# Kernel optimization log

Measured on AMD Instinct MI355X. Metric: run time of the kernel, lower is better.

Reference implementation:

```python
import jax, jax.numpy as jnp
import numpy as np

B, H, W, C = 8, 56, 56, 2048
NUM_HEADS = 8
WINDOW = 7  # partition/merge is identity for this per-token op; kept for documentation
D = C // NUM_HEADS  # 256


def setup_inputs() -> dict:
    key = jax.random.key(0)
    kx, kw = jax.random.split(key)
    x = jax.random.normal(kx, (B, H, W, C), dtype=jnp.float32)
    # per-head square weight, as in nn.Parameter(torch.randn(num_heads, d, d))
    weight = jax.random.normal(kw, (NUM_HEADS, D, D), dtype=jnp.float32)
    return {"x": x, "weight": weight}


def reference(x, weight):
    # Swin-style window partition -> per-head linear on each token -> window merge.
    # Partition and merge are exact inverse layout permutations, so the math
    # reduces to a per-token, per-head d x d matmul over the channel dim.
    b, h, w, c = x.shape
    n_heads, d, _ = weight.shape
    xh = x.reshape(b, h, w, n_heads, d)
    out = jnp.einsum('bhwnd,nde->bhwne', xh, weight)  # grouped small GEMM
    return out.reshape(b, h, w, c)
```

## Files before the change

### kernel.cpp

```cpp
#include <hip/hip_runtime.h>
#include <hip/hip_bf16.h>
#include <cstdint>

typedef __attribute__((ext_vector_type(8))) short v8s;
typedef __attribute__((ext_vector_type(4))) float v4f;

#define NUM_HEADS 8
#define D 256
#define CCH 2048
#define SEGS 64

__device__ __forceinline__ short f2bf(float f) {
  unsigned u = __builtin_bit_cast(unsigned, f);
  u = (u + 0x7FFFu + ((u >> 16) & 1u)) >> 16;
  return (short)u;
}

__global__ __launch_bounds__(256) void pack_w(const float* __restrict__ w,
                                              short* __restrict__ p) {
  int idx  = blockIdx.x * 256 + threadIdx.x;
  int lane = idx & 63;
  int j    = (idx >> 6) & 15;
  int s    = (idx >> 10) & 7;
  int head = idx >> 13;
  int n  = j * 16 + (lane & 15);
  int k0 = s * 32 + (lane >> 4) * 8;
  const float* src = w + head * 65536 + k0 * 256 + n;
  v8s v;
#pragma unroll
  for (int e = 0; e < 8; ++e) v[e] = f2bf(src[e * 256]);
  *reinterpret_cast<v8s*>(p + (size_t)idx * 8) = v;
}

typedef __attribute__((address_space(1))) const unsigned int GAS;
typedef __attribute__((address_space(3))) unsigned int LAS;

__global__ __launch_bounds__(512, 4) void grouped_mm(const float* __restrict__ x,
                                                     const short* __restrict__ pB,
                                                     float* __restrict__ out) {
  __shared__ alignas(16) char As[3][16384];
  const int tid  = threadIdx.x;
  const int wv   = tid >> 6;
  const int lane = tid & 63;
  const int head = blockIdx.x >> 6;
  const int seg  = blockIdx.x & 63;
  const int t0   = (seg < 32) ? seg * 25 : 800 + (seg - 32) * 24;
  const int nt   = (seg < 32) ? 25 : 24;

  const int arow = lane & 15;
  const int kg   = lane >> 4;

  v8s Bf0[8], Bf1[8];
  {
    const short* pb = pB + (size_t)head * 65536 + (size_t)lane * 8;
#pragma unroll
    for (int s = 0; s < 8; ++s) {
      Bf0[s] = *reinterpret_cast<const v8s*>(pb + (size_t)(s * 16 + 2 * wv)     * 512);
      Bf1[s] = *reinterpret_cast<const v8s*>(pb + (size_t)(s * 16 + 2 * wv + 1) * 512);
    }
  }

  const char* xbase = (const char*)(x + (size_t)head * D);

  auto stage = [&](int slot, int t) {
#pragma unroll
    for (int q = 0; q < 2; ++q) {
      const int r = 2 * wv + q;
      const unsigned lsw = ((unsigned)(lane * 16)) ^ (unsigned)((r & 7) << 4);
      const char* g = xbase + ((size_t)(t * 16 + r)) * (CCH * 4) + lsw;
      char* l = &As[0][0] + slot * 16384 + r * 1024;
      __builtin_amdgcn_global_load_lds((GAS*)g, (LAS*)l, 16, 0, 0);
    }
  };

  stage(0, t0);
  stage(1, t0 + 1);
  asm volatile("s_waitcnt vmcnt(2)" ::: "memory");
  __builtin_amdgcn_s_barrier();

  const unsigned rswz = (unsigned)((arow & 7) << 4);
  int cur = 0;

  for (int p = 0; p < nt; ++p) {
    int nslot = cur + 2; if (nslot >= 3) nslot -= 3;
    if (p + 2 < nt) stage(nslot, t0 + p + 2);

    const char* ar = &As[0][0] + cur * 16384 + arow * 1024;
    v4f acc0 = (v4f){0.f, 0.f, 0.f, 0.f};
    v4f acc1 = (v4f){0.f, 0.f, 0.f, 0.f};
#pragma unroll
    for (int s = 0; s < 8; ++s) {
      const unsigned q0 = ((unsigned)(s * 128 + kg * 32)) ^ rswz;
      v4f lo = *reinterpret_cast<const v4f*>(ar + q0);
      v4f hi = *reinterpret_cast<const v4f*>(ar + (q0 ^ 16u));
      v8s af;
#pragma unroll
      for (int e = 0; e < 4; ++e) {
        af[e]     = f2bf(lo[e]);
        af[4 + e] = f2bf(hi[e]);
      }
      acc0 = __builtin_amdgcn_mfma_f32_16x16x32_bf16(af, Bf0[s], acc0, 0, 0, 0);
      acc1 = __builtin_amdgcn_mfma_f32_16x16x32_bf16(af, Bf1[s], acc1, 0, 0, 0);
    }

    float* op = out + (size_t)((t0 + p) * 16 + kg * 4) * CCH
                    + head * D + wv * 32 + arow;
#pragma unroll
    for (int r = 0; r < 4; ++r) {
      op[(size_t)r * CCH]      = acc0[r];
      op[(size_t)r * CCH + 16] = acc1[r];
    }

    asm volatile("s_waitcnt vmcnt(10)" ::: "memory");
    __builtin_amdgcn_s_barrier();

    cur = cur + 1; if (cur >= 3) cur = 0;
  }
}

extern "C" void kernel_launch(void* const* d_in, const int* in_sizes, int n_in,
                              void* d_out, int out_size, void* d_ws, size_t ws_size,
                              hipStream_t stream) {
  const float* x = (const float*)d_in[0];
  const float* w = (const float*)d_in[1];
  float* out = (float*)d_out;
  short* packed = (short*)d_ws;

  pack_w<<<256, 256, 0, stream>>>(w, packed);
  grouped_mm<<<NUM_HEADS * SEGS, 512, 0, stream>>>(x, packed, out);
}
```

Baseline: 89.15 us.

## Stage activations through registers, convert to bf16 once before LDS

Replaces the direct global-to-LDS fp32 staging with register loads. Each thread converts its slice to bf16 once and writes it into a half-sized swizzled LDS tile. Before, every wave re-converted the same fp32 A tile, so this removes redundant conversions and halves LDS footprint and read traffic. In exchange, the prefetch now passes through VGPRs with a manually unrolled double-register pipeline. The vmcnt waits also cover outstanding output stores, which may add stalls in a kernel that is already near memory bandwidth.

```diff
diff --git a/kernel.cpp b/kernel.cpp
--- a/kernel.cpp
+++ b/kernel.cpp
@@ -32,13 +32,10 @@
   *reinterpret_cast<v8s*>(p + (size_t)idx * 8) = v;
 }
 
-typedef __attribute__((address_space(1))) const unsigned int GAS;
-typedef __attribute__((address_space(3))) unsigned int LAS;
-
 __global__ __launch_bounds__(512, 4) void grouped_mm(const float* __restrict__ x,
                                                      const short* __restrict__ pB,
                                                      float* __restrict__ out) {
-  __shared__ alignas(16) char As[3][16384];
+  __shared__ alignas(16) char As[3][8192];
   const int tid  = threadIdx.x;
   const int wv   = tid >> 6;
   const int lane = tid & 63;
@@ -47,8 +44,8 @@
   const int t0   = (seg < 32) ? seg * 25 : 800 + (seg - 32) * 24;
   const int nt   = (seg < 32) ? 25 : 24;
 
-  const int arow = lane & 15;
-  const int kg   = lane >> 4;
+  const int row = lane & 15;
+  const int kg  = lane >> 4;
 
   v8s Bf0[8], Bf1[8];
   {
@@ -60,62 +57,74 @@
     }
   }
 
-  const char* xbase = (const char*)(x + (size_t)head * D);
+  const int srow  = tid >> 5;
+  const int skseg = tid & 31;
+  const unsigned swoff = (unsigned)(srow * 512)
+                       + (((unsigned)(skseg * 16)) ^ ((unsigned)((srow & 7) << 4)));
+  const float* xbase = x + (size_t)head * D + (size_t)srow * CCH + skseg * 8;
 
-  auto stage = [&](int slot, int t) {
+  auto issue = [&](int t, v4f& g0, v4f& g1) {
+    const float* gp = xbase + (size_t)t * 16 * CCH;
+    g0 = *reinterpret_cast<const v4f*>(gp);
+    g1 = *reinterpret_cast<const v4f*>(gp + 4);
+  };
+  auto writeslot = [&](int slot, const v4f& g0, const v4f& g1) {
+    v8s wv8;
 #pragma unroll
-    for (int q = 0; q < 2; ++q) {
-      const int r = 2 * wv + q;
-      const unsigned lsw = ((unsigned)(lane * 16)) ^ (unsigned)((r & 7) << 4);
-      const char* g = xbase + ((size_t)(t * 16 + r)) * (CCH * 4) + lsw;
-      char* l = &As[0][0] + slot * 16384 + r * 1024;
-      __builtin_amdgcn_global_load_lds((GAS*)g, (LAS*)l, 16, 0, 0);
+    for (int e = 0; e < 4; ++e) {
+      wv8[e]     = f2bf(g0[e]);
+      wv8[4 + e] = f2bf(g1[e]);
     }
+    *reinterpret_cast<v8s*>(&As[0][0] + slot * 8192 + swoff) = wv8;
   };
 
-  stage(0, t0);
-  stage(1, t0 + 1);
-  asm volatile("s_waitcnt vmcnt(2)" ::: "memory");
-  __builtin_amdgcn_s_barrier();
+  const unsigned rsw = (unsigned)((row & 7) << 4);
 
-  const unsigned rswz = (unsigned)((arow & 7) << 4);
-  int cur = 0;
-
-  for (int p = 0; p < nt; ++p) {
-    int nslot = cur + 2; if (nslot >= 3) nslot -= 3;
-    if (p + 2 < nt) stage(nslot, t0 + p + 2);
-
-    const char* ar = &As[0][0] + cur * 16384 + arow * 1024;
+  auto compute = [&](int slot, int p) {
+    const char* ar = &As[0][0] + slot * 8192 + row * 512;
     v4f acc0 = (v4f){0.f, 0.f, 0.f, 0.f};
     v4f acc1 = (v4f){0.f, 0.f, 0.f, 0.f};
 #pragma unroll
     for (int s = 0; s < 8; ++s) {
-      const unsigned q0 = ((unsigned)(s * 128 + kg * 32)) ^ rswz;
-      v4f lo = *reinterpret_cast<const v4f*>(ar + q0);
-      v4f hi = *reinterpret_cast<const v4f*>(ar + (q0 ^ 16u));
-      v8s af;
-#pragma unroll
-      for (int e = 0; e < 4; ++e) {
-        af[e]     = f2bf(lo[e]);
-        af[4 + e] = f2bf(hi[e]);
-      }
+      const unsigned off = (((unsigned)((s * 4 + kg) * 16)) ^ rsw);
+      v8s af = *reinterpret_cast<const v8s*>(ar + off);
       acc0 = __builtin_amdgcn_mfma_f32_16x16x32_bf16(af, Bf0[s], acc0, 0, 0, 0);
       acc1 = __builtin_amdgcn_mfma_f32_16x16x32_bf16(af, Bf1[s], acc1, 0, 0, 0);
     }
-
     float* op = out + (size_t)((t0 + p) * 16 + kg * 4) * CCH
-                    + head * D + wv * 32 + arow;
+                    + head * D + wv * 32 + row;
 #pragma unroll
     for (int r = 0; r < 4; ++r) {
       op[(size_t)r * CCH]      = acc0[r];
       op[(size_t)r * CCH + 16] = acc1[r];
     }
+  };
 
-    asm volatile("s_waitcnt vmcnt(10)" ::: "memory");
-    __builtin_amdgcn_s_barrier();
+  v4f A0, A1, B0, B1;
+  issue(t0 + 0, A0, A1);
+  if (nt > 1) issue(t0 + 1, B0, B1);
+  asm volatile("s_waitcnt vmcnt(2)" ::: "memory");
+  writeslot(0, A0, A1);
+  asm volatile("s_waitcnt lgkmcnt(0)" ::: "memory");
+  __builtin_amdgcn_s_barrier();
 
-    cur = cur + 1; if (cur >= 3) cur = 0;
+#define BODY(p, GI0, GI1, GC0, GC1)                                        \
+  {                                                                        \
+    const int c = (p) % 3;                                                 \
+    int n1 = c + 1; if (n1 >= 3) n1 -= 3;                                  \
+    if ((p) + 2 < nt) issue(t0 + (p) + 2, GI0, GI1);                       \
+    asm volatile("s_waitcnt vmcnt(2)" ::: "memory");                       \
+    if ((p) + 1 < nt) writeslot(n1, GC0, GC1);                             \
+    compute(c, (p));                                                       \
+    asm volatile("s_waitcnt lgkmcnt(0)" ::: "memory");                     \
+    __builtin_amdgcn_s_barrier();                                          \
   }
+
+  for (int p = 0; p < nt; p += 2) {
+    BODY(p, A0, A1, B0, B1);
+    if (p + 1 < nt) BODY(p + 1, B0, B1, A0, A1);
+  }
+#undef BODY
 }
 
 extern "C" void kernel_launch(void* const* d_in, const int* in_sizes, int n_in,
```

Result: faster. 86.65 us (median of 2 runs) (-2.8%).
